# Optimization experiments

Measured on AMD Instinct MI355X. Metric: run time of the kernel, lower is better.

Reference implementation:

```python
import jax, jax.numpy as jnp
import numpy as np

DIM = 128
HEADS = 4
EPS = 1e-5


def setup_inputs() -> dict:
    key = jax.random.key(0)
    ks = jax.random.split(key, 14)
    B, N, C = 1, 256, DIM
    s = 1.0 / np.sqrt(C)
    inp = {
        'pair': jax.random.normal(ks[0], (B, N, N, C), dtype=jnp.float32),
        'Wq': jax.random.normal(ks[1], (C, C), dtype=jnp.float32) * s,
        'bq': jnp.zeros((C,), dtype=jnp.float32),
        'Wk': jax.random.normal(ks[2], (C, C), dtype=jnp.float32) * s,
        'bk': jnp.zeros((C,), dtype=jnp.float32),
        'Wv': jax.random.normal(ks[3], (C, C), dtype=jnp.float32) * s,
        'bv': jnp.zeros((C,), dtype=jnp.float32),
        'Wg': jax.random.normal(ks[4], (C, C), dtype=jnp.float32) * s,
        'bg': jnp.zeros((C,), dtype=jnp.float32),
        'Wo': jax.random.normal(ks[5], (C, C), dtype=jnp.float32) * s,
        'bo': jnp.zeros((C,), dtype=jnp.float32),
        'gamma': jnp.ones((C,), dtype=jnp.float32),
        'beta': jnp.zeros((C,), dtype=jnp.float32),
    }
    return inp


def _layernorm(x, gamma, beta):
    mu = jnp.mean(x, axis=-1, keepdims=True)
    var = jnp.mean(jnp.square(x - mu), axis=-1, keepdims=True)
    return (x - mu) * jax.lax.rsqrt(var + EPS) * gamma + beta


def reference(pair, Wq, bq, Wk, bk, Wv, bv, Wg, bg, Wo, bo, gamma, beta):
    B, N, _, C = pair.shape
    H = HEADS
    Ch = C // H
    scale = Ch ** (-0.5)
    # projections: nn.Linear is x @ W.T + b
    q = (pair @ Wq.T + bq).reshape(B, N, N, H, Ch)
    k = (pair @ Wk.T + bk).reshape(B, N, N, H, Ch)
    v = (pair @ Wv.T + bv).reshape(B, N, N, H, Ch)
    # per-row attention: logits [B,H,N(i),N(j),N(k)]
    attn = jnp.einsum('bijhc,bikhc->bhijk', q, k) * scale
    attn = jax.nn.softmax(attn, axis=-1)
    out = jnp.einsum('bhijk,bikhc->bijhc', attn, v).reshape(B, N, N, C)
    gate = jax.nn.sigmoid(pair @ Wg.T + bg)
    out = out * gate
    out = out @ Wo.T + bo
    return _layernorm(pair + out, gamma, beta)
```

## Files before the change

### kernel.cpp

```cpp
#include <hip/hip_runtime.h>
#include <hip/hip_bf16.h>

#define NN 256
#define CC 128
#define HH 4
#define CHD 32

typedef __attribute__((ext_vector_type(8))) short bf16x8;
typedef __attribute__((ext_vector_type(4))) short bf16x4;
typedef __attribute__((ext_vector_type(4))) float f32x4;

static __device__ __forceinline__ short f2bf(float f) {
  union { float f; unsigned u; } un; un.f = f;
  unsigned r = un.u + 0x7fff + ((un.u >> 16) & 1);
  return (short)(r >> 16);
}
static __device__ __forceinline__ float bf2f(short s) {
  union { unsigned u; float f; } un;
  un.u = ((unsigned)(unsigned short)s) << 16;
  return un.f;
}

__global__ void prep_kernel(const float* __restrict__ Wq, const float* __restrict__ Wk,
                            const float* __restrict__ Wv, const float* __restrict__ Wg,
                            const float* __restrict__ Wo, short* __restrict__ wpk)
{
  const int c = blockIdx.x * 256 + threadIdx.x;
  const int w = c >> 11;
  const int rem = c & 2047;
  const int t = rem >> 8;
  const int kc = (rem >> 6) & 3;
  const int lane = rem & 63;
  const float* W = (w == 0) ? Wq : (w == 1) ? Wk : (w == 2) ? Wv : (w == 3) ? Wg : Wo;
  const int row = t * 16 + (lane & 15);
  const int col = kc * 32 + (lane >> 4) * 8;
  const float* src = W + row * CC + col;
  bf16x8 b;
  #pragma unroll
  for (int j = 0; j < 8; ++j) b[j] = f2bf(src[j]);
  *(bf16x8*)(wpk + (size_t)c * 8) = b;
}

__global__ __launch_bounds__(256) void proj_kernel(
    const float* __restrict__ pair, const short* __restrict__ wpk,
    const float* __restrict__ bq, const float* __restrict__ bk,
    const float* __restrict__ bv, const float* __restrict__ bg,
    short* __restrict__ qo, short* __restrict__ ko,
    short* __restrict__ vo, short* __restrict__ go)
{
  const int wid  = threadIdx.x >> 6;
  const int lane = threadIdx.x & 63;
  const int g    = lane >> 4;
  const int t16  = lane & 15;

  const short* wsrc = wpk + (size_t)wid * 16384;
  bf16x8 wf[8][4];
  #pragma unroll
  for (int t = 0; t < 8; ++t)
    #pragma unroll
    for (int kc = 0; kc < 4; ++kc)
      wf[t][kc] = *(const bf16x8*)(wsrc + ((t*4 + kc)*64 + lane) * 8);

  const float* bias = (wid == 0) ? bq : (wid == 1) ? bk : (wid == 2) ? bv : bg;
  f32x4 bcol[8];
  #pragma unroll
  for (int t = 0; t < 8; ++t) bcol[t] = *(const f32x4*)(bias + t*16 + g*4);

  short* outp = (wid == 0) ? qo : (wid == 1) ? ko : (wid == 2) ? vo : go;
  const int row0 = blockIdx.x * 128;

  #pragma unroll 1
  for (int ch = 0; ch < 8; ++ch) {
    const int rbase = row0 + ch * 16;
    bf16x8 pf[4];
    #pragma unroll
    for (int kc = 0; kc < 4; ++kc) {
      const float* p = pair + (size_t)(rbase + t16) * CC + kc*32 + g*8;
      bf16x8 a;
      #pragma unroll
      for (int j = 0; j < 8; ++j) a[j] = f2bf(p[j]);
      pf[kc] = a;
    }
    f32x4 acc[8];
    #pragma unroll
    for (int t = 0; t < 8; ++t) acc[t] = f32x4{0.f, 0.f, 0.f, 0.f};
    #pragma unroll
    for (int kc = 0; kc < 4; ++kc)
      #pragma unroll
      for (int t = 0; t < 8; ++t)
        acc[t] = __builtin_amdgcn_mfma_f32_16x16x32_bf16(wf[t][kc], pf[kc], acc[t], 0, 0, 0);

    const size_t rowoff = (size_t)(rbase + t16) * CC;
    #pragma unroll
    for (int t = 0; t < 8; ++t) {
      f32x4 v;
      #pragma unroll
      for (int r = 0; r < 4; ++r) v[r] = acc[t][r] + bcol[t][r];
      if (wid == 3) {
        #pragma unroll
        for (int r = 0; r < 4; ++r) v[r] = 1.f / (1.f + __expf(-v[r]));
      }
      bf16x4 pk;
      #pragma unroll
      for (int r = 0; r < 4; ++r) pk[r] = f2bf(v[r]);
      *(bf16x4*)(outp + rowoff + t*16 + g*4) = pk;
    }
  }
}

__global__ __launch_bounds__(256) void attn_kernel(
    const short* __restrict__ qi, const short* __restrict__ ki,
    const short* __restrict__ vi, short* __restrict__ ao)
{
  __shared__ short Vt[32*264];
  __shared__ short Pl[4][16*264];

  const int bid  = blockIdx.x;
  const int i    = bid >> 2, h = bid & 3;
  const size_t pbase = (size_t)i * NN * CC + h * CHD;
  const int tid  = threadIdx.x;
  const int wid  = tid >> 6, lane = tid & 63;
  const int g    = lane >> 4, t16 = lane & 15;

  {
    const short* vr = vi + pbase + (size_t)tid * CC;
    #pragma unroll
    for (int u = 0; u < 4; ++u) {
      bf16x8 v8 = *(const bf16x8*)(vr + u*8);
      #pragma unroll
      for (int e = 0; e < 8; ++e)
        Vt[(u*8 + e)*264 + tid] = v8[e];
    }
  }
  __syncthreads();

  const float cs = 0.17677669529663689f * 1.4426950408889634f;

  #pragma unroll 1
  for (int c4 = 0; c4 < 4; ++c4) {
    const int q0 = wid*64 + c4*16;
    bf16x8 qf = *(const bf16x8*)(qi + pbase + (size_t)(q0 + t16)*CC + g*8);

    f32x4 s[16];
    #pragma unroll
    for (int t = 0; t < 16; ++t) {
      bf16x8 kf = *(const bf16x8*)(ki + pbase + (size_t)(t*16 + t16)*CC + g*8);
      s[t] = __builtin_amdgcn_mfma_f32_16x16x32_bf16(kf, qf, f32x4{0.f,0.f,0.f,0.f}, 0, 0, 0);
    }

    f32x4 m4 = s[0];
    #pragma unroll
    for (int t = 1; t < 16; ++t)
      #pragma unroll
      for (int r = 0; r < 4; ++r) m4[r] = fmaxf(m4[r], s[t][r]);
    float m = fmaxf(fmaxf(m4[0], m4[1]), fmaxf(m4[2], m4[3]));
    m = fmaxf(m, __shfl_xor(m, 16));
    m = fmaxf(m, __shfl_xor(m, 32));

    f32x4 s4 = f32x4{0.f,0.f,0.f,0.f};
    #pragma unroll
    for (int t = 0; t < 16; ++t) {
      f32x4 v = s[t];
      #pragma unroll
      for (int r = 0; r < 4; ++r) { v[r] = exp2f((v[r] - m) * cs); s4[r] += v[r]; }
      s[t] = v;
    }
    float sum = (s4[0] + s4[1]) + (s4[2] + s4[3]);
    sum += __shfl_xor(sum, 16);
    sum += __shfl_xor(sum, 32);
    const float sm = 1.f / sum;

    short* P = &Pl[wid][0];
    asm volatile("s_waitcnt lgkmcnt(0)" ::: "memory");
    #pragma unroll
    for (int t = 0; t < 16; ++t) {
      bf16x4 pk;
      #pragma unroll
      for (int r = 0; r < 4; ++r) pk[r] = f2bf(s[t][r]);
      *(bf16x4*)&P[t16*264 + t*16 + g*4] = pk;
    }
    asm volatile("s_waitcnt lgkmcnt(0)" ::: "memory");

    bf16x8 pa[8];
    #pragma unroll
    for (int kc = 0; kc < 8; ++kc)
      pa[kc] = *(const bf16x8*)&P[t16*264 + kc*32 + g*8];

    f32x4 o0 = f32x4{0.f,0.f,0.f,0.f};
    f32x4 o1 = f32x4{0.f,0.f,0.f,0.f};
    #pragma unroll
    for (int kc = 0; kc < 8; ++kc) {
      bf16x8 v0 = *(const bf16x8*)&Vt[t16*264 + kc*32 + g*8];
      bf16x8 v1 = *(const bf16x8*)&Vt[(16 + t16)*264 + kc*32 + g*8];
      o0 = __builtin_amdgcn_mfma_f32_16x16x32_bf16(v0, pa[kc], o0, 0, 0, 0);
      o1 = __builtin_amdgcn_mfma_f32_16x16x32_bf16(v1, pa[kc], o1, 0, 0, 0);
    }

    const size_t orow = pbase + (size_t)(q0 + t16) * CC;
    bf16x4 pk0, pk1;
    #pragma unroll
    for (int r = 0; r < 4; ++r) {
      pk0[r] = f2bf(o0[r] * sm);
      pk1[r] = f2bf(o1[r] * sm);
    }
    *(bf16x4*)(ao + orow + g*4)      = pk0;
    *(bf16x4*)(ao + orow + 16 + g*4) = pk1;
  }
}

__global__ __launch_bounds__(256) void out_kernel(
    const short* __restrict__ ai, const short* __restrict__ gi,
    const short* __restrict__ wpk_o, const float* __restrict__ bo,
    const float* __restrict__ pair, const float* __restrict__ gamma,
    const float* __restrict__ beta, float* __restrict__ out)
{
  __shared__ short Wl[16384];
  const int tid = threadIdx.x;
  const int wid = tid >> 6, lane = tid & 63;
  const int g = lane >> 4, t16 = lane & 15;

  #pragma unroll
  for (int it = 0; it < 8; ++it) {
    const int c = it*256 + tid;
    *(bf16x8*)&Wl[c*8] = *(const bf16x8*)(wpk_o + (size_t)c*8);
  }
  __syncthreads();

  const int m0 = blockIdx.x*64 + wid*16;
  const size_t rowoff = (size_t)(m0 + t16) * CC;

  bf16x8 xf[4];
  #pragma unroll
  for (int kc = 0; kc < 4; ++kc) {
    bf16x8 a8 = *(const bf16x8*)(ai + rowoff + kc*32 + g*8);
    bf16x8 g8 = *(const bf16x8*)(gi + rowoff + kc*32 + g*8);
    bf16x8 o;
    #pragma unroll
    for (int j = 0; j < 8; ++j) o[j] = f2bf(bf2f(a8[j]) * bf2f(g8[j]));
    xf[kc] = o;
  }

  f32x4 acc[8];
  #pragma unroll
  for (int t = 0; t < 8; ++t) acc[t] = f32x4{0.f,0.f,0.f,0.f};
  #pragma unroll
  for (int kc = 0; kc < 4; ++kc)
    #pragma unroll
    for (int t = 0; t < 8; ++t) {
      bf16x8 wfr = *(const bf16x8*)&Wl[((t*4 + kc)*64 + lane)*8];
      acc[t] = __builtin_amdgcn_mfma_f32_16x16x32_bf16(wfr, xf[kc], acc[t], 0, 0, 0);
    }

  float val[8][4];
  #pragma unroll
  for (int t = 0; t < 8; ++t) {
    f32x4 b4 = *(const f32x4*)(bo + t*16 + g*4);
    f32x4 p4 = *(const f32x4*)(pair + rowoff + t*16 + g*4);
    #pragma unroll
    for (int r = 0; r < 4; ++r) val[t][r] = acc[t][r] + b4[r] + p4[r];
  }
  float sum = 0.f;
  #pragma unroll
  for (int t = 0; t < 8; ++t)
    #pragma unroll
    for (int r = 0; r < 4; ++r) sum += val[t][r];
  sum += __shfl_xor(sum, 16); sum += __shfl_xor(sum, 32);
  const float mu = sum * (1.f/128.f);
  float sq = 0.f;
  #pragma unroll
  for (int t = 0; t < 8; ++t)
    #pragma unroll
    for (int r = 0; r < 4; ++r) { float d = val[t][r] - mu; sq += d*d; }
  sq += __shfl_xor(sq, 16); sq += __shfl_xor(sq, 32);
  const float rstd = rsqrtf(sq * (1.f/128.f) + 1e-5f);

  #pragma unroll
  for (int t = 0; t < 8; ++t) {
    f32x4 g4 = *(const f32x4*)(gamma + t*16 + g*4);
    f32x4 b4 = *(const f32x4*)(beta  + t*16 + g*4);
    f32x4 o4;
    #pragma unroll
    for (int r = 0; r < 4; ++r) o4[r] = (val[t][r] - mu) * rstd * g4[r] + b4[r];
    *(f32x4*)(out + rowoff + t*16 + g*4) = o4;
  }
}

extern "C" void kernel_launch(void* const* d_in, const int* in_sizes, int n_in,
                              void* d_out, int out_size, void* d_ws, size_t ws_size,
                              hipStream_t stream) {
  const float* pair  = (const float*)d_in[0];
  const float* Wq    = (const float*)d_in[1];
  const float* bq    = (const float*)d_in[2];
  const float* Wk    = (const float*)d_in[3];
  const float* bk    = (const float*)d_in[4];
  const float* Wv    = (const float*)d_in[5];
  const float* bv    = (const float*)d_in[6];
  const float* Wg    = (const float*)d_in[7];
  const float* bg    = (const float*)d_in[8];
  const float* Wo    = (const float*)d_in[9];
  const float* bo    = (const float*)d_in[10];
  const float* gamma = (const float*)d_in[11];
  const float* beta  = (const float*)d_in[12];
  float* out = (float*)d_out;

  short* wpk  = (short*)d_ws;
  short* q_ws = wpk + 81920;
  short* k_ws = q_ws + 8388608;
  short* v_ws = k_ws + 8388608;
  short* g_ws = v_ws + 8388608;
  short* a_ws = v_ws;

  hipLaunchKernelGGL(prep_kernel, dim3(40), dim3(256), 0, stream,
                     Wq, Wk, Wv, Wg, Wo, wpk);
  hipLaunchKernelGGL(proj_kernel, dim3(512), dim3(256), 0, stream,
                     pair, wpk, bq, bk, bv, bg, q_ws, k_ws, v_ws, g_ws);
  hipLaunchKernelGGL(attn_kernel, dim3(1024), dim3(256), 0, stream,
                     q_ws, k_ws, v_ws, a_ws);
  hipLaunchKernelGGL(out_kernel, dim3(1024), dim3(256), 0, stream,
                     a_ws, g_ws, wpk + 4*16384, bo, pair, gamma, beta, out);
}
```

Before: 208.0 us.

## Fuse projection, row attention and output projection into one per-row kernel

Replaces the three kernels (projection, attention, output+layernorm) with one kernel per pair row i, using 512 threads. K and V are projected straight into swizzled LDS, which removes their global round trip, while Q, gate and attention output still go through global scratch inside the kernel. The grid shrinks to 256 blocks using a large LDS allocation (160 KB). This lowers occupancy and parallelism, and the projection of the pair row is serialized before attention in each block.

```diff
diff --git a/kernel.cpp b/kernel.cpp
--- a/kernel.cpp
+++ b/kernel.cpp
@@ -3,8 +3,6 @@
 
 #define NN 256
 #define CC 128
-#define HH 4
-#define CHD 32
 
 typedef __attribute__((ext_vector_type(8))) short bf16x8;
 typedef __attribute__((ext_vector_type(4))) short bf16x4;
@@ -28,11 +26,11 @@
   const int c = blockIdx.x * 256 + threadIdx.x;
   const int w = c >> 11;
   const int rem = c & 2047;
-  const int t = rem >> 8;
+  const int nt = rem >> 8;
   const int kc = (rem >> 6) & 3;
   const int lane = rem & 63;
   const float* W = (w == 0) ? Wq : (w == 1) ? Wk : (w == 2) ? Wv : (w == 3) ? Wg : Wo;
-  const int row = t * 16 + (lane & 15);
+  const int row = nt * 16 + (lane & 15);
   const int col = kc * 32 + (lane >> 4) * 8;
   const float* src = W + row * CC + col;
   bf16x8 b;
@@ -41,247 +39,261 @@
   *(bf16x8*)(wpk + (size_t)c * 8) = b;
 }
 
-__global__ __launch_bounds__(256) void proj_kernel(
+__global__ __launch_bounds__(512, 2) void fused_kernel(
     const float* __restrict__ pair, const short* __restrict__ wpk,
     const float* __restrict__ bq, const float* __restrict__ bk,
     const float* __restrict__ bv, const float* __restrict__ bg,
-    short* __restrict__ qo, short* __restrict__ ko,
-    short* __restrict__ vo, short* __restrict__ go)
+    const float* __restrict__ bo, const float* __restrict__ gamma,
+    const float* __restrict__ beta,
+    short* __restrict__ Qg, short* __restrict__ Gg, short* __restrict__ Ag,
+    float* __restrict__ out)
 {
-  const int wid  = threadIdx.x >> 6;
-  const int lane = threadIdx.x & 63;
-  const int g    = lane >> 4;
-  const int t16  = lane & 15;
-
-  const short* wsrc = wpk + (size_t)wid * 16384;
-  bf16x8 wf[8][4];
-  #pragma unroll
-  for (int t = 0; t < 8; ++t)
-    #pragma unroll
-    for (int kc = 0; kc < 4; ++kc)
-      wf[t][kc] = *(const bf16x8*)(wsrc + ((t*4 + kc)*64 + lane) * 8);
-
-  const float* bias = (wid == 0) ? bq : (wid == 1) ? bk : (wid == 2) ? bv : bg;
-  f32x4 bcol[8];
-  #pragma unroll
-  for (int t = 0; t < 8; ++t) bcol[t] = *(const f32x4*)(bias + t*16 + g*4);
-
-  short* outp = (wid == 0) ? qo : (wid == 1) ? ko : (wid == 2) ? vo : go;
-  const int row0 = blockIdx.x * 128;
-
-  #pragma unroll 1
-  for (int ch = 0; ch < 8; ++ch) {
-    const int rbase = row0 + ch * 16;
-    bf16x8 pf[4];
-    #pragma unroll
-    for (int kc = 0; kc < 4; ++kc) {
-      const float* p = pair + (size_t)(rbase + t16) * CC + kc*32 + g*8;
-      bf16x8 a;
-      #pragma unroll
-      for (int j = 0; j < 8; ++j) a[j] = f2bf(p[j]);
-      pf[kc] = a;
-    }
-    f32x4 acc[8];
-    #pragma unroll
-    for (int t = 0; t < 8; ++t) acc[t] = f32x4{0.f, 0.f, 0.f, 0.f};
-    #pragma unroll
-    for (int kc = 0; kc < 4; ++kc)
-      #pragma unroll
-      for (int t = 0; t < 8; ++t)
-        acc[t] = __builtin_amdgcn_mfma_f32_16x16x32_bf16(wf[t][kc], pf[kc], acc[t], 0, 0, 0);
-
-    const size_t rowoff = (size_t)(rbase + t16) * CC;
-    #pragma unroll
-    for (int t = 0; t < 8; ++t) {
-      f32x4 v;
-      #pragma unroll
-      for (int r = 0; r < 4; ++r) v[r] = acc[t][r] + bcol[t][r];
-      if (wid == 3) {
-        #pragma unroll
-        for (int r = 0; r < 4; ++r) v[r] = 1.f / (1.f + __expf(-v[r]));
-      }
-      bf16x4 pk;
-      #pragma unroll
-      for (int r = 0; r < 4; ++r) pk[r] = f2bf(v[r]);
-      *(bf16x4*)(outp + rowoff + t*16 + g*4) = pk;
-    }
-  }
-}
-
-__global__ __launch_bounds__(256) void attn_kernel(
-    const short* __restrict__ qi, const short* __restrict__ ki,
-    const short* __restrict__ vi, short* __restrict__ ao)
-{
-  __shared__ short Vt[32*264];
-  __shared__ short Pl[4][16*264];
-
-  const int bid  = blockIdx.x;
-  const int i    = bid >> 2, h = bid & 3;
-  const size_t pbase = (size_t)i * NN * CC + h * CHD;
+  __shared__ short lds[81920];
+  short* Ksl = lds;
+  short* Vsl = lds + 32768;
+
+  const int i    = blockIdx.x;
   const int tid  = threadIdx.x;
   const int wid  = tid >> 6, lane = tid & 63;
   const int g    = lane >> 4, t16 = lane & 15;
+  const size_t prow = (size_t)i * NN * CC;
 
   {
-    const short* vr = vi + pbase + (size_t)tid * CC;
+    const int gm = wid >> 1;
+    const int rh = wid & 1;
+    const short* wsrc = wpk + (size_t)gm * 16384;
+    bf16x8 wf[8][4];
     #pragma unroll
-    for (int u = 0; u < 4; ++u) {
-      bf16x8 v8 = *(const bf16x8*)(vr + u*8);
-      #pragma unroll
-      for (int e = 0; e < 8; ++e)
-        Vt[(u*8 + e)*264 + tid] = v8[e];
+    for (int nt = 0; nt < 8; ++nt)
+      #pragma unroll
+      for (int kc = 0; kc < 4; ++kc)
+        wf[nt][kc] = *(const bf16x8*)(wsrc + ((nt*4 + kc)*64 + lane)*8);
+    const float* bias = (gm == 0) ? bq : (gm == 1) ? bk : (gm == 2) ? bv : bg;
+
+    #pragma unroll 1
+    for (int mc = 0; mc < 8; ++mc) {
+      const int m = rh*128 + mc*16 + t16;
+      bf16x8 pf[4];
+      #pragma unroll
+      for (int kc = 0; kc < 4; ++kc) {
+        const float* p = pair + prow + (size_t)m*CC + kc*32 + g*8;
+        bf16x8 a;
+        #pragma unroll
+        for (int j = 0; j < 8; ++j) a[j] = f2bf(p[j]);
+        pf[kc] = a;
+      }
+      f32x4 acc[8];
+      #pragma unroll
+      for (int nt = 0; nt < 8; ++nt) acc[nt] = f32x4{0.f,0.f,0.f,0.f};
+      #pragma unroll
+      for (int kc = 0; kc < 4; ++kc)
+        #pragma unroll
+        for (int nt = 0; nt < 8; ++nt)
+          acc[nt] = __builtin_amdgcn_mfma_f32_16x16x32_bf16(wf[nt][kc], pf[kc], acc[nt], 0, 0, 0);
+
+      if (gm == 0) {
+        #pragma unroll
+        for (int nt = 0; nt < 8; ++nt) {
+          f32x4 b4 = *(const f32x4*)(bias + nt*16 + g*4);
+          bf16x4 pk;
+          #pragma unroll
+          for (int r = 0; r < 4; ++r) pk[r] = f2bf(acc[nt][r] + b4[r]);
+          *(bf16x4*)(Qg + prow + (size_t)m*CC + nt*16 + g*4) = pk;
+        }
+      } else if (gm == 1) {
+        #pragma unroll
+        for (int nt = 0; nt < 8; ++nt) {
+          f32x4 b4 = *(const f32x4*)(bias + nt*16 + g*4);
+          bf16x4 pk;
+          #pragma unroll
+          for (int r = 0; r < 4; ++r) pk[r] = f2bf(acc[nt][r] + b4[r]);
+          *(bf16x4*)&Ksl[m*128 + ((nt*16 + g*4) ^ ((m & 7) << 3))] = pk;
+        }
+      } else if (gm == 2) {
+        #pragma unroll
+        for (int nt = 0; nt < 8; ++nt) {
+          f32x4 b4 = *(const f32x4*)(bias + nt*16 + g*4);
+          #pragma unroll
+          for (int r = 0; r < 4; ++r) {
+            const int ch = nt*16 + g*4 + r;
+            Vsl[ch*256 + (m ^ ((ch & 7) << 3))] = f2bf(acc[nt][r] + b4[r]);
+          }
+        }
+      } else {
+        #pragma unroll
+        for (int nt = 0; nt < 8; ++nt) {
+          f32x4 b4 = *(const f32x4*)(bias + nt*16 + g*4);
+          bf16x4 pk;
+          #pragma unroll
+          for (int r = 0; r < 4; ++r) {
+            float v = acc[nt][r] + b4[r];
+            pk[r] = f2bf(1.f / (1.f + __expf(-v)));
+          }
+          *(bf16x4*)(Gg + prow + (size_t)m*CC + nt*16 + g*4) = pk;
+        }
+      }
     }
   }
   __syncthreads();
 
-  const float cs = 0.17677669529663689f * 1.4426950408889634f;
-
-  #pragma unroll 1
-  for (int c4 = 0; c4 < 4; ++c4) {
-    const int q0 = wid*64 + c4*16;
-    bf16x8 qf = *(const bf16x8*)(qi + pbase + (size_t)(q0 + t16)*CC + g*8);
-
-    f32x4 s[16];
+  {
+    const int h  = wid >> 1;
+    const int qh = wid & 1;
+    short* Pw = lds + 65536 + wid*2048;
+
+    bf16x8 qf[8];
     #pragma unroll
-    for (int t = 0; t < 16; ++t) {
-      bf16x8 kf = *(const bf16x8*)(ki + pbase + (size_t)(t*16 + t16)*CC + g*8);
-      s[t] = __builtin_amdgcn_mfma_f32_16x16x32_bf16(kf, qf, f32x4{0.f,0.f,0.f,0.f}, 0, 0, 0);
+    for (int cc = 0; cc < 8; ++cc)
+      qf[cc] = *(const bf16x8*)(Qg + prow + (size_t)(qh*128 + cc*16 + t16)*CC + h*32 + g*8);
+
+    const float cs = 0.17677669529663689f * 1.4426950408889634f;
+    const int swzP = (t16 & 7) << 3;
+    const int ch0 = h*32 + t16, ch1 = ch0 + 16;
+    const int swzV = (ch0 & 7) << 3;
+
+    #pragma unroll 1
+    for (int cc = 0; cc < 8; ++cc) {
+      const int q0 = qh*128 + cc*16;
+
+      f32x4 s[16];
+      #pragma unroll
+      for (int t = 0; t < 16; ++t) {
+        const int row = t*16 + t16;
+        bf16x8 kf = *(const bf16x8*)&Ksl[row*128 + ((h*32 + g*8) ^ ((t16 & 7) << 3))];
+        s[t] = __builtin_amdgcn_mfma_f32_16x16x32_bf16(kf, qf[cc], f32x4{0.f,0.f,0.f,0.f}, 0, 0, 0);
+      }
+
+      f32x4 m4 = s[0];
+      #pragma unroll
+      for (int t = 1; t < 16; ++t)
+        #pragma unroll
+        for (int r = 0; r < 4; ++r) m4[r] = fmaxf(m4[r], s[t][r]);
+      float mx = fmaxf(fmaxf(m4[0], m4[1]), fmaxf(m4[2], m4[3]));
+      mx = fmaxf(mx, __shfl_xor(mx, 16));
+      mx = fmaxf(mx, __shfl_xor(mx, 32));
+
+      f32x4 s4 = f32x4{0.f,0.f,0.f,0.f};
+      #pragma unroll
+      for (int t = 0; t < 16; ++t) {
+        f32x4 v = s[t];
+        #pragma unroll
+        for (int r = 0; r < 4; ++r) { v[r] = exp2f((v[r] - mx) * cs); s4[r] += v[r]; }
+        s[t] = v;
+      }
+      float sum = (s4[0] + s4[1]) + (s4[2] + s4[3]);
+      sum += __shfl_xor(sum, 16);
+      sum += __shfl_xor(sum, 32);
+      const float sm = 1.f / sum;
+
+      f32x4 o0 = f32x4{0.f,0.f,0.f,0.f};
+      f32x4 o1 = f32x4{0.f,0.f,0.f,0.f};
+      #pragma unroll
+      for (int half = 0; half < 2; ++half) {
+        asm volatile("s_waitcnt lgkmcnt(0)" ::: "memory");
+        #pragma unroll
+        for (int tt = 0; tt < 8; ++tt) {
+          const int t = half*8 + tt;
+          bf16x4 pk;
+          #pragma unroll
+          for (int r = 0; r < 4; ++r) pk[r] = f2bf(s[t][r]);
+          *(bf16x4*)&Pw[t16*128 + ((tt*16 + g*4) ^ swzP)] = pk;
+        }
+        asm volatile("s_waitcnt lgkmcnt(0)" ::: "memory");
+
+        bf16x8 pa[4];
+        #pragma unroll
+        for (int kc = 0; kc < 4; ++kc)
+          pa[kc] = *(const bf16x8*)&Pw[t16*128 + ((kc*32 + g*8) ^ swzP)];
+
+        #pragma unroll
+        for (int kc = 0; kc < 4; ++kc) {
+          const int kb = half*128 + kc*32 + g*8;
+          bf16x8 v0 = *(const bf16x8*)&Vsl[ch0*256 + (kb ^ swzV)];
+          bf16x8 v1 = *(const bf16x8*)&Vsl[ch1*256 + (kb ^ swzV)];
+          o0 = __builtin_amdgcn_mfma_f32_16x16x32_bf16(v0, pa[kc], o0, 0, 0, 0);
+          o1 = __builtin_amdgcn_mfma_f32_16x16x32_bf16(v1, pa[kc], o1, 0, 0, 0);
+        }
+      }
+
+      const size_t ob = prow + (size_t)(q0 + t16)*CC + h*32;
+      bf16x4 pk0, pk1;
+      #pragma unroll
+      for (int r = 0; r < 4; ++r) { pk0[r] = f2bf(o0[r] * sm); pk1[r] = f2bf(o1[r] * sm); }
+      *(bf16x4*)(Ag + ob + g*4)      = pk0;
+      *(bf16x4*)(Ag + ob + 16 + g*4) = pk1;
     }
-
-    f32x4 m4 = s[0];
-    #pragma unroll
-    for (int t = 1; t < 16; ++t)
-      #pragma unroll
-      for (int r = 0; r < 4; ++r) m4[r] = fmaxf(m4[r], s[t][r]);
-    float m = fmaxf(fmaxf(m4[0], m4[1]), fmaxf(m4[2], m4[3]));
-    m = fmaxf(m, __shfl_xor(m, 16));
-    m = fmaxf(m, __shfl_xor(m, 32));
-
-    f32x4 s4 = f32x4{0.f,0.f,0.f,0.f};
-    #pragma unroll
-    for (int t = 0; t < 16; ++t) {
-      f32x4 v = s[t];
-      #pragma unroll
-      for (int r = 0; r < 4; ++r) { v[r] = exp2f((v[r] - m) * cs); s4[r] += v[r]; }
-      s[t] = v;
-    }
-    float sum = (s4[0] + s4[1]) + (s4[2] + s4[3]);
-    sum += __shfl_xor(sum, 16);
-    sum += __shfl_xor(sum, 32);
-    const float sm = 1.f / sum;
-
-    short* P = &Pl[wid][0];
-    asm volatile("s_waitcnt lgkmcnt(0)" ::: "memory");
-    #pragma unroll
-    for (int t = 0; t < 16; ++t) {
-      bf16x4 pk;
-      #pragma unroll
-      for (int r = 0; r < 4; ++r) pk[r] = f2bf(s[t][r]);
-      *(bf16x4*)&P[t16*264 + t*16 + g*4] = pk;
-    }
-    asm volatile("s_waitcnt lgkmcnt(0)" ::: "memory");
-
-    bf16x8 pa[8];
-    #pragma unroll
-    for (int kc = 0; kc < 8; ++kc)
-      pa[kc] = *(const bf16x8*)&P[t16*264 + kc*32 + g*8];
-
-    f32x4 o0 = f32x4{0.f,0.f,0.f,0.f};
-    f32x4 o1 = f32x4{0.f,0.f,0.f,0.f};
-    #pragma unroll
-    for (int kc = 0; kc < 8; ++kc) {
-      bf16x8 v0 = *(const bf16x8*)&Vt[t16*264 + kc*32 + g*8];
-      bf16x8 v1 = *(const bf16x8*)&Vt[(16 + t16)*264 + kc*32 + g*8];
-      o0 = __builtin_amdgcn_mfma_f32_16x16x32_bf16(v0, pa[kc], o0, 0, 0, 0);
-      o1 = __builtin_amdgcn_mfma_f32_16x16x32_bf16(v1, pa[kc], o1, 0, 0, 0);
-    }
-
-    const size_t orow = pbase + (size_t)(q0 + t16) * CC;
-    bf16x4 pk0, pk1;
-    #pragma unroll
-    for (int r = 0; r < 4; ++r) {
-      pk0[r] = f2bf(o0[r] * sm);
-      pk1[r] = f2bf(o1[r] * sm);
-    }
-    *(bf16x4*)(ao + orow + g*4)      = pk0;
-    *(bf16x4*)(ao + orow + 16 + g*4) = pk1;
-  }
-}
-
-__global__ __launch_bounds__(256) void out_kernel(
-    const short* __restrict__ ai, const short* __restrict__ gi,
-    const short* __restrict__ wpk_o, const float* __restrict__ bo,
-    const float* __restrict__ pair, const float* __restrict__ gamma,
-    const float* __restrict__ beta, float* __restrict__ out)
-{
-  __shared__ short Wl[16384];
-  const int tid = threadIdx.x;
-  const int wid = tid >> 6, lane = tid & 63;
-  const int g = lane >> 4, t16 = lane & 15;
-
-  #pragma unroll
-  for (int it = 0; it < 8; ++it) {
-    const int c = it*256 + tid;
-    *(bf16x8*)&Wl[c*8] = *(const bf16x8*)(wpk_o + (size_t)c*8);
   }
   __syncthreads();
 
-  const int m0 = blockIdx.x*64 + wid*16;
-  const size_t rowoff = (size_t)(m0 + t16) * CC;
-
-  bf16x8 xf[4];
-  #pragma unroll
-  for (int kc = 0; kc < 4; ++kc) {
-    bf16x8 a8 = *(const bf16x8*)(ai + rowoff + kc*32 + g*8);
-    bf16x8 g8 = *(const bf16x8*)(gi + rowoff + kc*32 + g*8);
-    bf16x8 o;
+  {
     #pragma unroll
-    for (int j = 0; j < 8; ++j) o[j] = f2bf(bf2f(a8[j]) * bf2f(g8[j]));
-    xf[kc] = o;
+    for (int it = 0; it < 4; ++it) {
+      const int c = it*512 + tid;
+      *(bf16x8*)&lds[c*8] = *(const bf16x8*)(wpk + 4*16384 + (size_t)c*8);
+    }
   }
-
-  f32x4 acc[8];
-  #pragma unroll
-  for (int t = 0; t < 8; ++t) acc[t] = f32x4{0.f,0.f,0.f,0.f};
-  #pragma unroll
-  for (int kc = 0; kc < 4; ++kc)
-    #pragma unroll
-    for (int t = 0; t < 8; ++t) {
-      bf16x8 wfr = *(const bf16x8*)&Wl[((t*4 + kc)*64 + lane)*8];
-      acc[t] = __builtin_amdgcn_mfma_f32_16x16x32_bf16(wfr, xf[kc], acc[t], 0, 0, 0);
+  __syncthreads();
+  {
+    #pragma unroll 1
+    for (int mc = 0; mc < 2; ++mc) {
+      const int m = wid*32 + mc*16 + t16;
+      const size_t rowoff = prow + (size_t)m * CC;
+
+      bf16x8 xf[4];
+      #pragma unroll
+      for (int kc = 0; kc < 4; ++kc) {
+        bf16x8 a8 = *(const bf16x8*)(Ag + rowoff + kc*32 + g*8);
+        bf16x8 g8 = *(const bf16x8*)(Gg + rowoff + kc*32 + g*8);
+        bf16x8 o;
+        #pragma unroll
+        for (int j = 0; j < 8; ++j) o[j] = f2bf(bf2f(a8[j]) * bf2f(g8[j]));
+        xf[kc] = o;
+      }
+
+      f32x4 acc[8];
+      #pragma unroll
+      for (int nt = 0; nt < 8; ++nt) acc[nt] = f32x4{0.f,0.f,0.f,0.f};
+      #pragma unroll
+      for (int kc = 0; kc < 4; ++kc)
+        #pragma unroll
+        for (int nt = 0; nt < 8; ++nt) {
+          bf16x8 wfr = *(const bf16x8*)&lds[((nt*4 + kc)*64 + lane)*8];
+          acc[nt] = __builtin_amdgcn_mfma_f32_16x16x32_bf16(wfr, xf[kc], acc[nt], 0, 0, 0);
+        }
+
+      float val[8][4];
+      #pragma unroll
+      for (int nt = 0; nt < 8; ++nt) {
+        f32x4 b4 = *(const f32x4*)(bo + nt*16 + g*4);
+        f32x4 p4 = *(const f32x4*)(pair + rowoff + nt*16 + g*4);
+        #pragma unroll
+        for (int r = 0; r < 4; ++r) val[nt][r] = acc[nt][r] + b4[r] + p4[r];
+      }
+      float sum = 0.f;
+      #pragma unroll
+      for (int nt = 0; nt < 8; ++nt)
+        #pragma unroll
+        for (int r = 0; r < 4; ++r) sum += val[nt][r];
+      sum += __shfl_xor(sum, 16); sum += __shfl_xor(sum, 32);
+      const float mu = sum * (1.f/128.f);
+      float sq = 0.f;
+      #pragma unroll
+      for (int nt = 0; nt < 8; ++nt)
+        #pragma unroll
+        for (int r = 0; r < 4; ++r) { float d = val[nt][r] - mu; sq += d*d; }
+      sq += __shfl_xor(sq, 16); sq += __shfl_xor(sq, 32);
+      const float rstd = rsqrtf(sq * (1.f/128.f) + 1e-5f);
+
+      #pragma unroll
+      for (int nt = 0; nt < 8; ++nt) {
+        f32x4 g4 = *(const f32x4*)(gamma + nt*16 + g*4);
+        f32x4 b4 = *(const f32x4*)(beta  + nt*16 + g*4);
+        f32x4 o4;
+        #pragma unroll
+        for (int r = 0; r < 4; ++r) o4[r] = (val[nt][r] - mu) * rstd * g4[r] + b4[r];
+        *(f32x4*)(out + rowoff + nt*16 + g*4) = o4;
+      }
     }
-
-  float val[8][4];
-  #pragma unroll
-  for (int t = 0; t < 8; ++t) {
-    f32x4 b4 = *(const f32x4*)(bo + t*16 + g*4);
-    f32x4 p4 = *(const f32x4*)(pair + rowoff + t*16 + g*4);
-    #pragma unroll
-    for (int r = 0; r < 4; ++r) val[t][r] = acc[t][r] + b4[r] + p4[r];
-  }
-  float sum = 0.f;
-  #pragma unroll
-  for (int t = 0; t < 8; ++t)
-    #pragma unroll
-    for (int r = 0; r < 4; ++r) sum += val[t][r];
-  sum += __shfl_xor(sum, 16); sum += __shfl_xor(sum, 32);
-  const float mu = sum * (1.f/128.f);
-  float sq = 0.f;
-  #pragma unroll
-  for (int t = 0; t < 8; ++t)
-    #pragma unroll
-    for (int r = 0; r < 4; ++r) { float d = val[t][r] - mu; sq += d*d; }
-  sq += __shfl_xor(sq, 16); sq += __shfl_xor(sq, 32);
-  const float rstd = rsqrtf(sq * (1.f/128.f) + 1e-5f);
-
-  #pragma unroll
-  for (int t = 0; t < 8; ++t) {
-    f32x4 g4 = *(const f32x4*)(gamma + t*16 + g*4);
-    f32x4 b4 = *(const f32x4*)(beta  + t*16 + g*4);
-    f32x4 o4;
-    #pragma unroll
-    for (int r = 0; r < 4; ++r) o4[r] = (val[t][r] - mu) * rstd * g4[r] + b4[r];
-    *(f32x4*)(out + rowoff + t*16 + g*4) = o4;
   }
 }
 
@@ -305,17 +317,12 @@
 
   short* wpk  = (short*)d_ws;
   short* q_ws = wpk + 81920;
-  short* k_ws = q_ws + 8388608;
-  short* v_ws = k_ws + 8388608;
-  short* g_ws = v_ws + 8388608;
-  short* a_ws = v_ws;
+  short* g_ws = q_ws + 8388608;
+  short* a_ws = g_ws + 8388608;
 
   hipLaunchKernelGGL(prep_kernel, dim3(40), dim3(256), 0, stream,
                      Wq, Wk, Wv, Wg, Wo, wpk);
-  hipLaunchKernelGGL(proj_kernel, dim3(512), dim3(256), 0, stream,
-                     pair, wpk, bq, bk, bv, bg, q_ws, k_ws, v_ws, g_ws);
-  hipLaunchKernelGGL(attn_kernel, dim3(1024), dim3(256), 0, stream,
-                     q_ws, k_ws, v_ws, a_ws);
-  hipLaunchKernelGGL(out_kernel, dim3(1024), dim3(256), 0, stream,
-                     a_ws, g_ws, wpk + 4*16384, bo, pair, gamma, beta, out);
-}
+  hipLaunchKernelGGL(fused_kernel, dim3(256), dim3(512), 0, stream,
+                     pair, wpk, bq, bk, bv, bg, bo, gamma, beta,
+                     q_ws, g_ws, a_ws, out);
+}
```

Result: slower. 245.7 us (+18.1%).
